# Kernel tuning notes

Measured on AMD Instinct MI355X. Metric: run time of the kernel, lower is better.

Reference implementation:

```python
import jax, jax.numpy as jnp
import numpy as np

B, M, N = 16, 1024, 4096
CIN, HID = 67, 128  # in_channels+3, hid_channels
BN_EPS = 1e-5


def setup_inputs() -> dict:
    key = jax.random.key(0)
    ks = jax.random.split(key, 13)
    inp = {
        "cent_feat": jax.random.normal(ks[0], (B, M, CIN), dtype=jnp.float32),
        "feat": jax.random.normal(ks[1], (B, N, CIN), dtype=jnp.float32),
        "mask": jax.random.uniform(ks[2], (B, M, N), dtype=jnp.float32),
        # Conv1d(k=1, bias=False) weights, xavier-normal-ish scale
        "Wq": jax.random.normal(ks[3], (HID, CIN), dtype=jnp.float32) * np.float32(np.sqrt(2.0 / (HID + CIN))),
        "Wk": jax.random.normal(ks[4], (HID, CIN), dtype=jnp.float32) * np.float32(np.sqrt(2.0 / (HID + CIN))),
        # BatchNorm1d params (inference form)
        "gq": jax.random.uniform(ks[5], (HID,), dtype=jnp.float32, minval=0.5, maxval=1.5),
        "bq": jax.random.normal(ks[6], (HID,), dtype=jnp.float32) * 0.1,
        "mq": jax.random.normal(ks[7], (HID,), dtype=jnp.float32) * 0.1,
        "vq": jax.random.uniform(ks[8], (HID,), dtype=jnp.float32, minval=0.5, maxval=1.5),
        "gk": jax.random.uniform(ks[9], (HID,), dtype=jnp.float32, minval=0.5, maxval=1.5),
        "bk": jax.random.normal(ks[10], (HID,), dtype=jnp.float32) * 0.1,
        "mk": jax.random.normal(ks[11], (HID,), dtype=jnp.float32) * 0.1,
        "vk": jax.random.uniform(ks[12], (HID,), dtype=jnp.float32, minval=0.5, maxval=1.5),
    }
    return inp


def _bn(x, g, b, m, v):
    # BatchNorm1d over channel dim (last axis here), inference form
    return (x - m) * (g / jnp.sqrt(v + BN_EPS)) + b


def _l1_normalize(x, axis):
    # torch F.normalize(p=1): x / max(||x||_1, 1e-12)
    return x / jnp.maximum(jnp.sum(jnp.abs(x), axis=axis, keepdims=True), 1e-12)


def reference(cent_feat, feat, mask, Wq, Wk, gq, bq, mq, vq, gk, bk, mk, vk):
    # Conv1x1 (1x1 conv = channel matmul) + BN, no activation
    q = _bn(jnp.einsum("bmc,hc->bmh", cent_feat, Wq), gq, bq, mq, vq)  # [B,M,H]
    k = _bn(jnp.einsum("bnc,hc->bnh", feat, Wk), gk, bk, mk, vk)       # [B,N,H]
    adj = jnp.einsum("bmh,bnh->bmn", q, k)                              # [B,M,N]
    adj = jnp.where(mask < 1e-9, jnp.float32(-1e9), adj)
    adj = jax.nn.softmax(adj, axis=-1)
    adj = jnp.sqrt(mask + 1e-9) * jnp.sqrt(adj + 1e-9) - 1e-9
    adj = _l1_normalize(adj, axis=1)
    adj = _l1_normalize(adj, axis=-1)
    return adj
```

## Files before the change

kernel.cpp:

```cpp
#include <hip/hip_runtime.h>
#include <hip/hip_fp16.h>

#define B_ 16
#define M_ 1024
#define N_ 4096
#define H_ 128
#define CIN_ 67

typedef _Float16 half8 __attribute__((ext_vector_type(8)));
typedef _Float16 half4_t __attribute__((ext_vector_type(4)));
typedef float f32x4 __attribute__((ext_vector_type(4)));

#define SPA 104

__global__ __launch_bounds__(256) void k_embed(
    const float* __restrict__ cent, const float* __restrict__ feat,
    const float* __restrict__ Wq, const float* __restrict__ Wk,
    const float* __restrict__ gq, const float* __restrict__ bq,
    const float* __restrict__ mq, const float* __restrict__ vq,
    const float* __restrict__ gk, const float* __restrict__ bk,
    const float* __restrict__ mk, const float* __restrict__ vk,
    __half* __restrict__ q16, __half* __restrict__ k16)
{
  __shared__ __align__(16) __half al[128 * SPA];
  __shared__ __align__(16) __half wl[128 * SPA];
  __shared__ float scl[128], shl[128];

  const int tid = threadIdx.x;
  const int wg  = blockIdx.x;
  const bool isq = (wg < 128);
  const int row0 = isq ? wg * 128 : (wg - 128) * 128;
  const float* in = isq ? cent : feat;
  const float* W  = isq ? Wq : Wk;
  const float* g  = isq ? gq : gk;
  const float* bb = isq ? bq : bk;
  const float* mm = isq ? mq : mk;
  const float* vv = isq ? vq : vk;
  __half* outp = isq ? q16 : k16;

  for (int i = tid; i < 128 * 29; i += 256) {
    int r = i / 29, c = 67 + (i - r * 29);
    al[r * SPA + c] = __float2half(0.f);
    wl[r * SPA + c] = __float2half(0.f);
  }
  for (int i = tid; i < 128 * CIN_; i += 256) {
    int r = i / CIN_, c = i - r * CIN_;
    al[r * SPA + c] = __float2half(in[(size_t)row0 * CIN_ + i]);
    wl[r * SPA + c] = __float2half(W[i]);
  }
  if (tid < 128) {
    float s = g[tid] * rsqrtf(vv[tid] + 1e-5f);
    scl[tid] = s;
    shl[tid] = bb[tid] - mm[tid] * s;
  }
  __syncthreads();

  const int lane = tid & 63, wv = tid >> 6;
  const int col = lane & 15, quad = lane >> 4;

  f32x4 acc[2][8];
#pragma unroll
  for (int ms = 0; ms < 2; ++ms)
#pragma unroll
    for (int ns = 0; ns < 8; ++ns) acc[ms][ns] = (f32x4){0.f, 0.f, 0.f, 0.f};

#pragma unroll
  for (int kk = 0; kk < 3; ++kk) {
    half8 af[2], bf[8];
#pragma unroll
    for (int ms = 0; ms < 2; ++ms)
      af[ms] = *(const half8*)&al[(wv * 32 + ms * 16 + col) * SPA + kk * 32 + quad * 8];
#pragma unroll
    for (int ns = 0; ns < 8; ++ns)
      bf[ns] = *(const half8*)&wl[(ns * 16 + col) * SPA + kk * 32 + quad * 8];
#pragma unroll
    for (int ms = 0; ms < 2; ++ms)
#pragma unroll
      for (int ns = 0; ns < 8; ++ns)
        acc[ms][ns] = __builtin_amdgcn_mfma_f32_16x16x32_f16(af[ms], bf[ns], acc[ms][ns], 0, 0, 0);
  }

#pragma unroll
  for (int ms = 0; ms < 2; ++ms)
#pragma unroll
    for (int reg = 0; reg < 4; ++reg) {
      int r = wv * 32 + ms * 16 + quad * 4 + reg;
#pragma unroll
      for (int ns = 0; ns < 8; ++ns) {
        int h = ns * 16 + col;
        float v = acc[ms][ns][reg] * scl[h] + shl[h];
        outp[(size_t)(row0 + r) * H_ + h] = __float2half(v);
      }
    }
}

#define SPB 136

__global__ __launch_bounds__(256, 2) void k_attn1(
    const __half* __restrict__ q16, const __half* __restrict__ k16,
    float* __restrict__ pmax, float* __restrict__ psum)
{
  __shared__ __align__(16) __half qa[128 * SPB];
  __shared__ __align__(16) __half ka[128 * SPB];

  const int tid = threadIdx.x;
  const int b = blockIdx.z, mt = blockIdx.y, nt = blockIdx.x;
  const int m0 = mt * 128, n0 = nt * 128;

  {
    const uint4* srcq = (const uint4*)(q16 + ((size_t)(b * M_) + m0) * H_);
    const uint4* srck = (const uint4*)(k16 + ((size_t)(b * N_) + n0) * H_);
    for (int i = tid; i < 2048; i += 256) {
      int r = i >> 4, c = i & 15;
      *(uint4*)&qa[r * SPB + c * 8] = srcq[i];
      *(uint4*)&ka[r * SPB + c * 8] = srck[i];
    }
  }
  __syncthreads();

  const int lane = tid & 63, wv = tid >> 6;
  const int col = lane & 15, quad = lane >> 4;

  f32x4 acc[2][8];
#pragma unroll
  for (int ms = 0; ms < 2; ++ms)
#pragma unroll
    for (int ns = 0; ns < 8; ++ns) acc[ms][ns] = (f32x4){0.f, 0.f, 0.f, 0.f};

#pragma unroll
  for (int kk = 0; kk < 4; ++kk) {
    half8 af[2], bf[8];
#pragma unroll
    for (int ms = 0; ms < 2; ++ms)
      af[ms] = *(const half8*)&qa[(wv * 32 + ms * 16 + col) * SPB + kk * 32 + quad * 8];
#pragma unroll
    for (int ns = 0; ns < 8; ++ns)
      bf[ns] = *(const half8*)&ka[(ns * 16 + col) * SPB + kk * 32 + quad * 8];
#pragma unroll
    for (int ms = 0; ms < 2; ++ms)
#pragma unroll
      for (int ns = 0; ns < 8; ++ns)
        acc[ms][ns] = __builtin_amdgcn_mfma_f32_16x16x32_f16(af[ms], bf[ns], acc[ms][ns], 0, 0, 0);
  }

#pragma unroll
  for (int ms = 0; ms < 2; ++ms)
#pragma unroll
    for (int reg = 0; reg < 4; ++reg) {
      const int m = m0 + wv * 32 + ms * 16 + quad * 4 + reg;
      float mx = -3e38f;
#pragma unroll
      for (int ns = 0; ns < 8; ++ns) mx = fmaxf(mx, acc[ms][ns][reg]);
      mx = fmaxf(mx, __shfl_xor(mx, 1));
      mx = fmaxf(mx, __shfl_xor(mx, 2));
      mx = fmaxf(mx, __shfl_xor(mx, 4));
      mx = fmaxf(mx, __shfl_xor(mx, 8));
      float s = 0.f;
#pragma unroll
      for (int ns = 0; ns < 8; ++ns) s += __expf(acc[ms][ns][reg] - mx);
      s += __shfl_xor(s, 1);
      s += __shfl_xor(s, 2);
      s += __shfl_xor(s, 4);
      s += __shfl_xor(s, 8);
      if (col == 0) {
        size_t rg = (size_t)b * M_ + m;
        pmax[rg * 32 + nt] = mx;
        psum[rg * 32 + nt] = s;
      }
    }
}

__global__ __launch_bounds__(256) void k_comb(
    const float* __restrict__ pmax, const float* __restrict__ psum,
    float* __restrict__ Mr, float* __restrict__ iZ)
{
  int r = blockIdx.x * 256 + threadIdx.x;
  float mx = -3e38f;
#pragma unroll
  for (int i = 0; i < 32; ++i) mx = fmaxf(mx, pmax[(size_t)r * 32 + i]);
  float z = 0.f;
#pragma unroll
  for (int i = 0; i < 32; ++i)
    z += psum[(size_t)r * 32 + i] * __expf(pmax[(size_t)r * 32 + i] - mx);
  Mr[r] = mx;
  iZ[r] = 1.f / z;
}

__global__ __launch_bounds__(256, 2) void k_attn3(
    const __half* __restrict__ q16, const __half* __restrict__ k16,
    const float* __restrict__ mask,
    const float* __restrict__ Mr, const float* __restrict__ iZ,
    __half* __restrict__ t16, float* __restrict__ colsum)
{
  __shared__ __align__(16) __half qa[128 * SPB];
  __shared__ __align__(16) __half ka[128 * SPB];
  __shared__ float MrL[128], iZL[128];

  const int tid = threadIdx.x;
  const int b = blockIdx.z, mt = blockIdx.y, nt = blockIdx.x;
  const int m0 = mt * 128, n0 = nt * 128;

  {
    const uint4* srcq = (const uint4*)(q16 + ((size_t)(b * M_) + m0) * H_);
    const uint4* srck = (const uint4*)(k16 + ((size_t)(b * N_) + n0) * H_);
    for (int i = tid; i < 2048; i += 256) {
      int r = i >> 4, c = i & 15;
      *(uint4*)&qa[r * SPB + c * 8] = srcq[i];
      *(uint4*)&ka[r * SPB + c * 8] = srck[i];
    }
  }
  if (tid < 128) {
    MrL[tid] = Mr[b * M_ + m0 + tid];
    iZL[tid] = iZ[b * M_ + m0 + tid];
  }
  __syncthreads();

  const int lane = tid & 63, wv = tid >> 6;
  const int col = lane & 15, quad = lane >> 4;

  f32x4 acc[2][8];
#pragma unroll
  for (int ms = 0; ms < 2; ++ms)
#pragma unroll
    for (int ns = 0; ns < 8; ++ns) acc[ms][ns] = (f32x4){0.f, 0.f, 0.f, 0.f};

#pragma unroll
  for (int kk = 0; kk < 4; ++kk) {
    half8 af[2], bf[8];
#pragma unroll
    for (int ms = 0; ms < 2; ++ms)
      af[ms] = *(const half8*)&ka[(wv * 32 + ms * 16 + col) * SPB + kk * 32 + quad * 8];
#pragma unroll
    for (int ns = 0; ns < 8; ++ns)
      bf[ns] = *(const half8*)&qa[(ns * 16 + col) * SPB + kk * 32 + quad * 8];
#pragma unroll
    for (int ms = 0; ms < 2; ++ms)
#pragma unroll
      for (int ns = 0; ns < 8; ++ns)
        acc[ms][ns] = __builtin_amdgcn_mfma_f32_16x16x32_f16(af[ms], bf[ns], acc[ms][ns], 0, 0, 0);
  }

  float cs[8];
#pragma unroll
  for (int i = 0; i < 8; ++i) cs[i] = 0.f;

#pragma unroll
  for (int msN = 0; msN < 2; ++msN) {
    const int nb = n0 + wv * 32 + msN * 16 + quad * 4;
#pragma unroll
    for (int nsm = 0; nsm < 8; ++nsm) {
      const int ml = nsm * 16 + col;
      const int m = m0 + ml;
      const float mr = MrL[ml], z = iZL[ml];
      const size_t base = ((size_t)b * M_ + m) * N_ + nb;
      const float4 mv = *(const float4*)&mask[base];
      half4_t h;
#pragma unroll
      for (int reg = 0; reg < 4; ++reg) {
        float mvv = (reg == 0) ? mv.x : (reg == 1) ? mv.y : (reg == 2) ? mv.z : mv.w;
        float x = acc[msN][nsm][reg];
        x = (mvv < 1e-9f) ? -1e9f : x;
        float p = __expf(x - mr) * z;
        float t = sqrtf((mvv + 1e-9f) * (p + 1e-9f)) - 1e-9f;
        h[reg] = (_Float16)t;
        cs[msN * 4 + reg] += t;
      }
      *(half4_t*)&t16[base] = h;
    }
  }
#pragma unroll
  for (int i = 0; i < 8; ++i) {
    cs[i] += __shfl_xor(cs[i], 1);
    cs[i] += __shfl_xor(cs[i], 2);
    cs[i] += __shfl_xor(cs[i], 4);
    cs[i] += __shfl_xor(cs[i], 8);
  }
  if (col == 0) {
#pragma unroll
    for (int i = 0; i < 8; ++i) {
      int n = n0 + wv * 32 + (i >> 2) * 16 + quad * 4 + (i & 3);
      atomicAdd(&colsum[(size_t)b * N_ + n], cs[i]);
    }
  }
}

__global__ __launch_bounds__(256) void k_norm(
    const __half* __restrict__ t16, float* __restrict__ out,
    const float* __restrict__ colsum)
{
  const int row = blockIdx.x;
  const int b = row >> 10;
  const half4_t* t4 = (const half4_t*)(t16 + (size_t)row * N_);
  float4* o4 = (float4*)(out + (size_t)row * N_);
  const float4* c4 = (const float4*)(colsum + (size_t)b * N_);
  const int tid = threadIdx.x;

  float4 u[4];
  float s = 0.f;
#pragma unroll
  for (int j = 0; j < 4; ++j) {
    int idx = tid + 256 * j;
    half4_t h = t4[idx];
    float4 c = c4[idx];
    u[j].x = (float)h[0] / fmaxf(c.x, 1e-12f);
    u[j].y = (float)h[1] / fmaxf(c.y, 1e-12f);
    u[j].z = (float)h[2] / fmaxf(c.z, 1e-12f);
    u[j].w = (float)h[3] / fmaxf(c.w, 1e-12f);
    s += u[j].x + u[j].y + u[j].z + u[j].w;
  }
  s += __shfl_xor(s, 1);
  s += __shfl_xor(s, 2);
  s += __shfl_xor(s, 4);
  s += __shfl_xor(s, 8);
  s += __shfl_xor(s, 16);
  s += __shfl_xor(s, 32);
  __shared__ float red[4];
  if ((tid & 63) == 0) red[tid >> 6] = s;
  __syncthreads();
  float tot = red[0] + red[1] + red[2] + red[3];
  float inv = 1.f / fmaxf(tot, 1e-12f);
#pragma unroll
  for (int j = 0; j < 4; ++j) {
    int idx = tid + 256 * j;
    float4 v = u[j];
    v.x *= inv; v.y *= inv; v.z *= inv; v.w *= inv;
    o4[idx] = v;
  }
}

extern "C" void kernel_launch(void* const* d_in, const int* in_sizes, int n_in,
                              void* d_out, int out_size, void* d_ws, size_t ws_size,
                              hipStream_t stream) {
  const float* cent = (const float*)d_in[0];
  const float* feat = (const float*)d_in[1];
  const float* mask = (const float*)d_in[2];
  const float* Wq = (const float*)d_in[3];
  const float* Wk = (const float*)d_in[4];
  const float* gq = (const float*)d_in[5];
  const float* bq = (const float*)d_in[6];
  const float* mq = (const float*)d_in[7];
  const float* vq = (const float*)d_in[8];
  const float* gk = (const float*)d_in[9];
  const float* bk = (const float*)d_in[10];
  const float* mk = (const float*)d_in[11];
  const float* vk = (const float*)d_in[12];
  float* out = (float*)d_out;

  char* ws = (char*)d_ws;
  __half* q16  = (__half*)(ws + 0);
  __half* k16  = (__half*)(ws + 4194304);
  __half* t16  = (__half*)(ws + 20971520);
  float* pmax  = (float*)(ws + 155189248);
  float* psum  = (float*)(ws + 157286400);
  float* Mr    = (float*)(ws + 159383552);
  float* iZ    = (float*)(ws + 159449088);
  float* colsum= (float*)(ws + 159514624);

  hipMemsetAsync(colsum, 0, (size_t)B_ * N_ * sizeof(float), stream);

  k_embed<<<640, 256, 0, stream>>>(cent, feat, Wq, Wk, gq, bq, mq, vq,
                                   gk, bk, mk, vk, q16, k16);

  dim3 gg(N_ / 128, M_ / 128, B_);
  k_attn1<<<gg, 256, 0, stream>>>(q16, k16, pmax, psum);
  k_comb<<<64, 256, 0, stream>>>(pmax, psum, Mr, iZ);
  k_attn3<<<gg, 256, 0, stream>>>(q16, k16, mask, Mr, iZ, t16, colsum);
  k_norm<<<B_ * M_, 256, 0, stream>>>(t16, out, colsum);
}
```

Baseline: 646.8 us.

## Drop row-max softmax stabilization and accumulate partition sums via atomics

Result: faster. 613.7 us (-5.1%).

```diff
diff --git a/kernel.cpp b/kernel.cpp
--- a/kernel.cpp
+++ b/kernel.cpp
@@ -98,10 +98,99 @@
 
 __global__ __launch_bounds__(256, 2) void k_attn1(
     const __half* __restrict__ q16, const __half* __restrict__ k16,
-    float* __restrict__ pmax, float* __restrict__ psum)
+    float* __restrict__ Z)
 {
   __shared__ __align__(16) __half qa[128 * SPB];
   __shared__ __align__(16) __half ka[128 * SPB];
+
+  const int tid = threadIdx.x;
+  const int b = blockIdx.z, mt = blockIdx.y, ns = blockIdx.x;
+  const int m0 = mt * 128;
+
+  {
+    const uint4* srcq = (const uint4*)(q16 + ((size_t)(b * M_) + m0) * H_);
+    for (int i = tid; i < 2048; i += 256) {
+      int r = i >> 4, c = i & 15;
+      *(uint4*)&qa[r * SPB + c * 8] = srcq[i];
+    }
+  }
+
+  const int lane = tid & 63, wv = tid >> 6;
+  const int col = lane & 15, quad = lane >> 4;
+
+  float zacc[8];
+#pragma unroll
+  for (int i = 0; i < 8; ++i) zacc[i] = 0.f;
+
+  for (int t = 0; t < 8; ++t) {
+    if (t) __syncthreads();
+    const int n0 = (ns * 8 + t) * 128;
+    {
+      const uint4* srck = (const uint4*)(k16 + ((size_t)(b * N_) + n0) * H_);
+      for (int i = tid; i < 2048; i += 256) {
+        int r = i >> 4, c = i & 15;
+        *(uint4*)&ka[r * SPB + c * 8] = srck[i];
+      }
+    }
+    __syncthreads();
+
+    f32x4 acc[2][8];
+#pragma unroll
+    for (int ms = 0; ms < 2; ++ms)
+#pragma unroll
+      for (int nb = 0; nb < 8; ++nb) acc[ms][nb] = (f32x4){0.f, 0.f, 0.f, 0.f};
+
+#pragma unroll
+    for (int kk = 0; kk < 4; ++kk) {
+      half8 af[2], bf[8];
+#pragma unroll
+      for (int ms = 0; ms < 2; ++ms)
+        af[ms] = *(const half8*)&qa[(wv * 32 + ms * 16 + col) * SPB + kk * 32 + quad * 8];
+#pragma unroll
+      for (int nb = 0; nb < 8; ++nb)
+        bf[nb] = *(const half8*)&ka[(nb * 16 + col) * SPB + kk * 32 + quad * 8];
+#pragma unroll
+      for (int ms = 0; ms < 2; ++ms)
+#pragma unroll
+        for (int nb = 0; nb < 8; ++nb)
+          acc[ms][nb] = __builtin_amdgcn_mfma_f32_16x16x32_f16(af[ms], bf[nb], acc[ms][nb], 0, 0, 0);
+    }
+
+#pragma unroll
+    for (int ms = 0; ms < 2; ++ms)
+#pragma unroll
+      for (int reg = 0; reg < 4; ++reg) {
+        float s = 0.f;
+#pragma unroll
+        for (int nb = 0; nb < 8; ++nb) s += __expf(acc[ms][nb][reg]);
+        zacc[ms * 4 + reg] += s;
+      }
+  }
+
+#pragma unroll
+  for (int i = 0; i < 8; ++i) {
+    zacc[i] += __shfl_xor(zacc[i], 1);
+    zacc[i] += __shfl_xor(zacc[i], 2);
+    zacc[i] += __shfl_xor(zacc[i], 4);
+    zacc[i] += __shfl_xor(zacc[i], 8);
+  }
+  if (col == 0) {
+#pragma unroll
+    for (int i = 0; i < 8; ++i) {
+      int m = m0 + wv * 32 + (i >> 2) * 16 + quad * 4 + (i & 3);
+      atomicAdd(&Z[(size_t)b * M_ + m], zacc[i]);
+    }
+  }
+}
+
+__global__ __launch_bounds__(256, 2) void k_attn3(
+    const __half* __restrict__ q16, const __half* __restrict__ k16,
+    const float* __restrict__ mask, const float* __restrict__ Z,
+    __half* __restrict__ t16, float* __restrict__ colsum)
+{
+  __shared__ __align__(16) __half qa[128 * SPB];
+  __shared__ __align__(16) __half ka[128 * SPB];
+  __shared__ float lnZL[128];
 
   const int tid = threadIdx.x;
   const int b = blockIdx.z, mt = blockIdx.y, nt = blockIdx.x;
@@ -116,103 +205,7 @@
       *(uint4*)&ka[r * SPB + c * 8] = srck[i];
     }
   }
-  __syncthreads();
-
-  const int lane = tid & 63, wv = tid >> 6;
-  const int col = lane & 15, quad = lane >> 4;
-
-  f32x4 acc[2][8];
-#pragma unroll
-  for (int ms = 0; ms < 2; ++ms)
-#pragma unroll
-    for (int ns = 0; ns < 8; ++ns) acc[ms][ns] = (f32x4){0.f, 0.f, 0.f, 0.f};
-
-#pragma unroll
-  for (int kk = 0; kk < 4; ++kk) {
-    half8 af[2], bf[8];
-#pragma unroll
-    for (int ms = 0; ms < 2; ++ms)
-      af[ms] = *(const half8*)&qa[(wv * 32 + ms * 16 + col) * SPB + kk * 32 + quad * 8];
-#pragma unroll
-    for (int ns = 0; ns < 8; ++ns)
-      bf[ns] = *(const half8*)&ka[(ns * 16 + col) * SPB + kk * 32 + quad * 8];
-#pragma unroll
-    for (int ms = 0; ms < 2; ++ms)
-#pragma unroll
-      for (int ns = 0; ns < 8; ++ns)
-        acc[ms][ns] = __builtin_amdgcn_mfma_f32_16x16x32_f16(af[ms], bf[ns], acc[ms][ns], 0, 0, 0);
-  }
-
-#pragma unroll
-  for (int ms = 0; ms < 2; ++ms)
-#pragma unroll
-    for (int reg = 0; reg < 4; ++reg) {
-      const int m = m0 + wv * 32 + ms * 16 + quad * 4 + reg;
-      float mx = -3e38f;
-#pragma unroll
-      for (int ns = 0; ns < 8; ++ns) mx = fmaxf(mx, acc[ms][ns][reg]);
-      mx = fmaxf(mx, __shfl_xor(mx, 1));
-      mx = fmaxf(mx, __shfl_xor(mx, 2));
-      mx = fmaxf(mx, __shfl_xor(mx, 4));
-      mx = fmaxf(mx, __shfl_xor(mx, 8));
-      float s = 0.f;
-#pragma unroll
-      for (int ns = 0; ns < 8; ++ns) s += __expf(acc[ms][ns][reg] - mx);
-      s += __shfl_xor(s, 1);
-      s += __shfl_xor(s, 2);
-      s += __shfl_xor(s, 4);
-      s += __shfl_xor(s, 8);
-      if (col == 0) {
-        size_t rg = (size_t)b * M_ + m;
-        pmax[rg * 32 + nt] = mx;
-        psum[rg * 32 + nt] = s;
-      }
-    }
-}
-
-__global__ __launch_bounds__(256) void k_comb(
-    const float* __restrict__ pmax, const float* __restrict__ psum,
-    float* __restrict__ Mr, float* __restrict__ iZ)
-{
-  int r = blockIdx.x * 256 + threadIdx.x;
-  float mx = -3e38f;
-#pragma unroll
-  for (int i = 0; i < 32; ++i) mx = fmaxf(mx, pmax[(size_t)r * 32 + i]);
-  float z = 0.f;
-#pragma unroll
-  for (int i = 0; i < 32; ++i)
-    z += psum[(size_t)r * 32 + i] * __expf(pmax[(size_t)r * 32 + i] - mx);
-  Mr[r] = mx;
-  iZ[r] = 1.f / z;
-}
-
-__global__ __launch_bounds__(256, 2) void k_attn3(
-    const __half* __restrict__ q16, const __half* __restrict__ k16,
-    const float* __restrict__ mask,
-    const float* __restrict__ Mr, const float* __restrict__ iZ,
-    __half* __restrict__ t16, float* __restrict__ colsum)
-{
-  __shared__ __align__(16) __half qa[128 * SPB];
-  __shared__ __align__(16) __half ka[128 * SPB];
-  __shared__ float MrL[128], iZL[128];
-
-  const int tid = threadIdx.x;
-  const int b = blockIdx.z, mt = blockIdx.y, nt = blockIdx.x;
-  const int m0 = mt * 128, n0 = nt * 128;
-
-  {
-    const uint4* srcq = (const uint4*)(q16 + ((size_t)(b * M_) + m0) * H_);
-    const uint4* srck = (const uint4*)(k16 + ((size_t)(b * N_) + n0) * H_);
-    for (int i = tid; i < 2048; i += 256) {
-      int r = i >> 4, c = i & 15;
-      *(uint4*)&qa[r * SPB + c * 8] = srcq[i];
-      *(uint4*)&ka[r * SPB + c * 8] = srck[i];
-    }
-  }
-  if (tid < 128) {
-    MrL[tid] = Mr[b * M_ + m0 + tid];
-    iZL[tid] = iZ[b * M_ + m0 + tid];
-  }
+  if (tid < 128) lnZL[tid] = __logf(Z[b * M_ + m0 + tid]);
   __syncthreads();
 
   const int lane = tid & 63, wv = tid >> 6;
@@ -251,7 +244,7 @@
     for (int nsm = 0; nsm < 8; ++nsm) {
       const int ml = nsm * 16 + col;
       const int m = m0 + ml;
-      const float mr = MrL[ml], z = iZL[ml];
+      const float lz = lnZL[ml];
       const size_t base = ((size_t)b * M_ + m) * N_ + nb;
       const float4 mv = *(const float4*)&mask[base];
       half4_t h;
@@ -260,7 +253,7 @@
         float mvv = (reg == 0) ? mv.x : (reg == 1) ? mv.y : (reg == 2) ? mv.z : mv.w;
         float x = acc[msN][nsm][reg];
         x = (mvv < 1e-9f) ? -1e9f : x;
-        float p = __expf(x - mr) * z;
+        float p = __expf(x - lz);
         float t = sqrtf((mvv + 1e-9f) * (p + 1e-9f)) - 1e-9f;
         h[reg] = (_Float16)t;
         cs[msN * 4 + reg] += t;
@@ -350,20 +343,18 @@
   __half* q16  = (__half*)(ws + 0);
   __half* k16  = (__half*)(ws + 4194304);
   __half* t16  = (__half*)(ws + 20971520);
-  float* pmax  = (float*)(ws + 155189248);
-  float* psum  = (float*)(ws + 157286400);
-  float* Mr    = (float*)(ws + 159383552);
-  float* iZ    = (float*)(ws + 159449088);
-  float* colsum= (float*)(ws + 159514624);
-
-  hipMemsetAsync(colsum, 0, (size_t)B_ * N_ * sizeof(float), stream);
+  float* colsum= (float*)(ws + 155189248);
+  float* Zr    = (float*)(ws + 155451392);
+
+  hipMemsetAsync(colsum, 0, 262144 + 65536, stream);
 
   k_embed<<<640, 256, 0, stream>>>(cent, feat, Wq, Wk, gq, bq, mq, vq,
                                    gk, bk, mk, vk, q16, k16);
 
-  dim3 gg(N_ / 128, M_ / 128, B_);
-  k_attn1<<<gg, 256, 0, stream>>>(q16, k16, pmax, psum);
-  k_comb<<<64, 256, 0, stream>>>(pmax, psum, Mr, iZ);
-  k_attn3<<<gg, 256, 0, stream>>>(q16, k16, mask, Mr, iZ, t16, colsum);
+  dim3 g1(4, 8, 16);
+  k_attn1<<<g1, 256, 0, stream>>>(q16, k16, Zr);
+
+  dim3 g3(N_ / 128, M_ / 128, B_);
+  k_attn3<<<g3, 256, 0, stream>>>(q16, k16, mask, Zr, t16, colsum);
   k_norm<<<B_ * M_, 256, 0, stream>>>(t16, out, colsum);
 }
```
